# Kernel optimization log

Hardware: AMD Instinct MI355X
Metric: run time of the kernel (lower is better)

Reference implementation:

```python
import jax, jax.numpy as jnp
import numpy as np

DIM = 2048
ORDER = 4
L_MAX = 2048
BATCH = 4  # must equal ORDER due to broadcast in the original module
SEQ = 2048


def setup_inputs() -> dict:
    key = jax.random.key(0)
    k1, k2 = jax.random.split(key)
    x = jax.random.normal(k1, (BATCH, DIM, SEQ), dtype=jnp.float32)
    kernel = jax.random.normal(k2, (ORDER, DIM, L_MAX), dtype=jnp.float32) * 0.02
    bias = jnp.zeros((DIM,), dtype=jnp.float32)
    return {"x": x, "kernel": kernel, "bias": bias}


def reference(x, kernel, bias):
    # x: (B, dim, L); kernel: (order, dim, l_max); B == order by broadcast
    seq_len = x.shape[-1]
    n = 2 * seq_len  # zero-padded FFT length for linear (causal) convolution
    x_fft = jnp.fft.rfft(x, n=n, axis=-1)            # (B, dim, n//2+1) complex
    kernel_fft = jnp.fft.rfft(kernel, n=n, axis=-1)  # (order, dim, n//2+1)
    y_fft = x_fft * kernel_fft                       # broadcast: B == order
    y = jnp.fft.irfft(y_fft, n=n, axis=-1)[:, :, :seq_len]
    return y + x + bias[None, :, None]
```

## Files before the change

kernel.cpp:

```cpp
#include <hip/hip_runtime.h>

typedef __attribute__((ext_vector_type(8)))  short short8;
typedef __attribute__((ext_vector_type(16))) float f32x16;

#define SEQ    2048
#define XPITCH 20
#define XROWS  96
#define XSZ    (XROWS * XPITCH)
#define KSZ    1044
#define WSZ    (XSZ + 2 * KSZ)

__device__ inline unsigned int pack_bf16_2(float lo, float hi) {
    unsigned int ul = __float_as_uint(lo);
    unsigned int uh = __float_as_uint(hi);
    ul = (ul + 0x7fffu + ((ul >> 16) & 1u)) >> 16;
    uh = (uh + 0x7fffu + ((uh >> 16) & 1u)) >> 16;
    return (ul & 0xffffu) | (uh << 16);
}

#define MFMA(A, B, C) __builtin_amdgcn_mfma_f32_32x32x16_bf16( \
    __builtin_bit_cast(short8, A), __builtin_bit_cast(short8, B), C, 0, 0, 0)

__global__ __launch_bounds__(256, 2)
void hyena_mfma(const float* __restrict__ x, const float* __restrict__ kern,
                const float* __restrict__ bias, float* __restrict__ out)
{
    __shared__ __align__(16) unsigned int lds[4 * WSZ];

    const int tid = threadIdx.x;
    const int wid = tid >> 6;
    const int l   = tid & 63;
    const int n   = l & 31;
    const int hi  = l >> 5;
    const int row = blockIdx.x * 4 + wid;
    const size_t rb = (size_t)row * SEQ;

    unsigned int* xld  = lds + wid * WSZ;
    unsigned int* bufA = xld + XSZ;
    unsigned int* bufB = bufA + KSZ;

    #pragma unroll
    for (int it = 0; it < 16; ++it) {
        const int e = it * 128 + 2 * l;
        float2 v = *(const float2*)&x[rb + e];
        const int R = 32 + (e >> 5);
        xld[R * XPITCH + ((e & 31) >> 1)] = pack_bf16_2(v.x, v.y);
    }
    #pragma unroll
    for (int it = 0; it < 10; ++it) xld[it * 64 + l] = 0u;

    #pragma unroll
    for (int it = 0; it < 16; ++it) {
        const int j = it * 128 + 2 * l;
        float2 v = *(const float2*)&kern[rb + (2046 - j)];
        bufA[j >> 1] = pack_bf16_2(v.y, v.x);
    }
    if (l < 20) bufA[1024 + l] = 0u;
    __syncthreads();

    #pragma unroll
    for (int it = 0; it < 17; ++it) {
        const int m = it * 64 + l;
        if (m < 1040) {
            unsigned int a = bufA[m], b = bufA[m + 1];
            bufB[m] = (a >> 16) | (b << 16);
        }
    }
    __syncthreads();

    int iA = (32 + n) * XPITCH + 4 * hi;
    const int base0 = 2047 - n + 8 * hi;
    const unsigned int* kb;
    int iK;
    if (base0 & 1) { kb = bufB; iK = (base0 - 1) >> 1; }
    else           { kb = bufA; iK = base0 >> 1; }

    f32x16 acc0 = {}, acc1a = {}, acc1b = {};

    #pragma unroll 4
    for (int r = 0; r < 32; ++r) {
        const uint4 a00 = *(const uint4*)(xld + iA);
        const uint4 a01 = *(const uint4*)(xld + iA + 8);
        const uint4 a10 = *(const uint4*)(xld + iA + 32 * XPITCH);
        const uint4 a11 = *(const uint4*)(xld + iA + 32 * XPITCH + 8);
        uint4 b00, b01, b10, b11;
        b00.x = kb[iK];       b00.y = kb[iK + 1];   b00.z = kb[iK + 2];   b00.w = kb[iK + 3];
        b01.x = kb[iK + 8];   b01.y = kb[iK + 9];   b01.z = kb[iK + 10];  b01.w = kb[iK + 11];
        b10.x = kb[iK - 512]; b10.y = kb[iK - 511]; b10.z = kb[iK - 510]; b10.w = kb[iK - 509];
        b11.x = kb[iK - 504]; b11.y = kb[iK - 503]; b11.z = kb[iK - 502]; b11.w = kb[iK - 501];

        acc0  = MFMA(a00, b00, acc0);
        acc0  = MFMA(a01, b01, acc0);
        acc1a = MFMA(a10, b00, acc1a);
        acc1a = MFMA(a11, b01, acc1a);
        acc1b = MFMA(a00, b10, acc1b);
        acc1b = MFMA(a01, b11, acc1b);

        iA -= XPITCH;
        iK -= 16;
    }

    const float bv = bias[row & 2047];
    #pragma unroll
    for (int mt = 0; mt < 2; ++mt) {
        #pragma unroll
        for (int t = 0; t < 16; ++t) {
            const int rloc = (t & 3) + 8 * (t >> 2) + 4 * hi;
            const int p = mt * 32 + rloc;
            const unsigned int w = xld[(32 + p) * XPITCH + (n >> 1)];
            const float xr = __uint_as_float((n & 1) ? (w & 0xffff0000u) : (w << 16));
            const float a = mt ? (acc1a[t] + acc1b[t]) : acc0[t];
            out[rb + (size_t)p * 32 + n] = a + xr + bv;
        }
    }
}

extern "C" void kernel_launch(void* const* d_in, const int* in_sizes, int n_in,
                              void* d_out, int out_size, void* d_ws, size_t ws_size,
                              hipStream_t stream) {
    const float* x    = (const float*)d_in[0];
    const float* kern = (const float*)d_in[1];
    const float* bias = (const float*)d_in[2];
    float* out = (float*)d_out;

    hipLaunchKernelGGL(hyena_mfma, dim3(2048), dim3(256), 0, stream,
                       x, kern, bias, out);
}
```

Before: 69.54 us.

## Drop shifted kernel copy, realign B operands via funnel shifts, raise occupancy

Removes the second, half-element-shifted copy of the reversed kernel and the 32 zero-padding rows of x from shared memory. Misaligned B fragments are now built in registers with 64-bit funnel shifts and selects, and zero A rows come from a small shared zero region chosen per lane. This cuts per-block shared memory and one barrier, so launch bounds are raised to 4 blocks per CU. The cost is extra ALU work and more LDS loads per MFMA step in the inner loop, and lower register headroom at the higher occupancy.

```diff
diff --git a/kernel.cpp b/kernel.cpp
--- a/kernel.cpp
+++ b/kernel.cpp
@@ -2,17 +2,19 @@
 
 typedef __attribute__((ext_vector_type(8)))  short short8;
 typedef __attribute__((ext_vector_type(16))) float f32x16;
+typedef unsigned int uint;
+typedef unsigned long long ull;
 
 #define SEQ    2048
 #define XPITCH 20
-#define XROWS  96
-#define XSZ    (XROWS * XPITCH)
-#define KSZ    1044
-#define WSZ    (XSZ + 2 * KSZ)
+#define XSZ    (64 * XPITCH)
+#define KSZ    1040
+#define WSZ    (XSZ + KSZ)
+#define LDSU   (4 * WSZ + 16)
 
-__device__ inline unsigned int pack_bf16_2(float lo, float hi) {
-    unsigned int ul = __float_as_uint(lo);
-    unsigned int uh = __float_as_uint(hi);
+__device__ inline uint pack_bf16_2(float lo, float hi) {
+    uint ul = __float_as_uint(lo);
+    uint uh = __float_as_uint(hi);
     ul = (ul + 0x7fffu + ((ul >> 16) & 1u)) >> 16;
     uh = (uh + 0x7fffu + ((uh >> 16) & 1u)) >> 16;
     return (ul & 0xffffu) | (uh << 16);
@@ -21,11 +23,23 @@
 #define MFMA(A, B, C) __builtin_amdgcn_mfma_f32_32x32x16_bf16( \
     __builtin_bit_cast(short8, A), __builtin_bit_cast(short8, B), C, 0, 0, 0)
 
-__global__ __launch_bounds__(256, 2)
+__device__ inline uint fnl(uint h, uint l, uint sh) {
+    return (uint)((((ull)h << 32) | l) >> sh);
+}
+
+#define SEL4(W0, W1, W2, W3, W4, W5, OUT) {                          \
+    uint t0 = c2 ? (W1) : (W0), t1 = c2 ? (W2) : (W1),               \
+         t2 = c2 ? (W3) : (W2), t3 = c2 ? (W4) : (W3),               \
+         t4 = c2 ? (W5) : (W4);                                      \
+    OUT.x = fnl(t1, t0, sh); OUT.y = fnl(t2, t1, sh);                \
+    OUT.z = fnl(t3, t2, sh); OUT.w = fnl(t4, t3, sh); }
+
+__global__ __launch_bounds__(256, 4)
 void hyena_mfma(const float* __restrict__ x, const float* __restrict__ kern,
                 const float* __restrict__ bias, float* __restrict__ out)
 {
-    __shared__ __align__(16) unsigned int lds[4 * WSZ];
+    __shared__ __align__(16) uint lds[LDSU];
+    char* ldsb = (char*)lds;
 
     const int tid = threadIdx.x;
     const int wid = tid >> 6;
@@ -35,69 +49,69 @@
     const int row = blockIdx.x * 4 + wid;
     const size_t rb = (size_t)row * SEQ;
 
-    unsigned int* xld  = lds + wid * WSZ;
-    unsigned int* bufA = xld + XSZ;
-    unsigned int* bufB = bufA + KSZ;
+    uint* xw = lds + wid * WSZ;
+    uint* kw = xw + XSZ;
 
     #pragma unroll
     for (int it = 0; it < 16; ++it) {
         const int e = it * 128 + 2 * l;
         float2 v = *(const float2*)&x[rb + e];
-        const int R = 32 + (e >> 5);
-        xld[R * XPITCH + ((e & 31) >> 1)] = pack_bf16_2(v.x, v.y);
+        xw[(e >> 5) * XPITCH + ((e & 31) >> 1)] = pack_bf16_2(v.x, v.y);
     }
-    #pragma unroll
-    for (int it = 0; it < 10; ++it) xld[it * 64 + l] = 0u;
-
     #pragma unroll
     for (int it = 0; it < 16; ++it) {
         const int j = it * 128 + 2 * l;
         float2 v = *(const float2*)&kern[rb + (2046 - j)];
-        bufA[j >> 1] = pack_bf16_2(v.y, v.x);
+        kw[j >> 1] = pack_bf16_2(v.y, v.x);
     }
-    if (l < 20) bufA[1024 + l] = 0u;
+    if (l < 16) kw[1024 + l] = 0u;
+    if (tid < 16) lds[4 * WSZ + tid] = 0u;
     __syncthreads();
 
-    #pragma unroll
-    for (int it = 0; it < 17; ++it) {
-        const int m = it * 64 + l;
-        if (m < 1040) {
-            unsigned int a = bufA[m], b = bufA[m + 1];
-            bufB[m] = (a >> 16) | (b << 16);
-        }
-    }
-    __syncthreads();
-
-    int iA = (32 + n) * XPITCH + 4 * hi;
-    const int base0 = 2047 - n + 8 * hi;
-    const unsigned int* kb;
-    int iK;
-    if (base0 & 1) { kb = bufB; iK = (base0 - 1) >> 1; }
-    else           { kb = bufA; iK = base0 >> 1; }
+    const int st00 = 2047 - n + 8 * hi;
+    const bool c2  = (st00 & 2) != 0;
+    const uint sh  = (uint)(st00 & 1) << 4;
+    int vk  = (wid * WSZ + XSZ) * 4 + ((st00 & ~3) << 1) - 2048;
+    int va2 = wid * WSZ * 4 + (n + 32) * 80 + 16 * hi;
+    const int vz = 4 * WSZ * 4 + 16 * hi;
 
     f32x16 acc0 = {}, acc1a = {}, acc1b = {};
 
-    #pragma unroll 4
+    #pragma unroll 2
     for (int r = 0; r < 32; ++r) {
-        const uint4 a00 = *(const uint4*)(xld + iA);
-        const uint4 a01 = *(const uint4*)(xld + iA + 8);
-        const uint4 a10 = *(const uint4*)(xld + iA + 32 * XPITCH);
-        const uint4 a11 = *(const uint4*)(xld + iA + 32 * XPITCH + 8);
-        uint4 b00, b01, b10, b11;
-        b00.x = kb[iK];       b00.y = kb[iK + 1];   b00.z = kb[iK + 2];   b00.w = kb[iK + 3];
-        b01.x = kb[iK + 8];   b01.y = kb[iK + 9];   b01.z = kb[iK + 10];  b01.w = kb[iK + 11];
-        b10.x = kb[iK - 512]; b10.y = kb[iK - 511]; b10.z = kb[iK - 510]; b10.w = kb[iK - 509];
-        b11.x = kb[iK - 504]; b11.y = kb[iK - 503]; b11.z = kb[iK - 502]; b11.w = kb[iK - 501];
+        const int va = (n >= r) ? (va2 - 2560) : vz;
+        const uint4 a00 = *(const uint4*)(ldsb + va);
+        const uint4 a01 = *(const uint4*)(ldsb + va + 32);
+        const uint4 a10 = *(const uint4*)(ldsb + va2);
+        const uint4 a11 = *(const uint4*)(ldsb + va2 + 32);
 
-        acc0  = MFMA(a00, b00, acc0);
-        acc0  = MFMA(a01, b01, acc0);
-        acc1a = MFMA(a10, b00, acc1a);
-        acc1a = MFMA(a11, b01, acc1a);
-        acc1b = MFMA(a00, b10, acc1b);
-        acc1b = MFMA(a01, b11, acc1b);
+        uint2 q0, q1, q2;
+        uint4 B;
+        q0 = *(const uint2*)(ldsb + vk + 2048);
+        q1 = *(const uint2*)(ldsb + vk + 2056);
+        q2 = *(const uint2*)(ldsb + vk + 2064);
+        SEL4(q0.x, q0.y, q1.x, q1.y, q2.x, q2.y, B);
+        acc0  = MFMA(a00, B, acc0);
+        acc1a = MFMA(a10, B, acc1a);
+        q0 = *(const uint2*)(ldsb + vk + 2080);
+        q1 = *(const uint2*)(ldsb + vk + 2088);
+        q2 = *(const uint2*)(ldsb + vk + 2096);
+        SEL4(q0.x, q0.y, q1.x, q1.y, q2.x, q2.y, B);
+        acc0  = MFMA(a01, B, acc0);
+        acc1a = MFMA(a11, B, acc1a);
+        q0 = *(const uint2*)(ldsb + vk);
+        q1 = *(const uint2*)(ldsb + vk + 8);
+        q2 = *(const uint2*)(ldsb + vk + 16);
+        SEL4(q0.x, q0.y, q1.x, q1.y, q2.x, q2.y, B);
+        acc1b = MFMA(a00, B, acc1b);
+        q0 = *(const uint2*)(ldsb + vk + 32);
+        q1 = *(const uint2*)(ldsb + vk + 40);
+        q2 = *(const uint2*)(ldsb + vk + 48);
+        SEL4(q0.x, q0.y, q1.x, q1.y, q2.x, q2.y, B);
+        acc1b = MFMA(a01, B, acc1b);
 
-        iA -= XPITCH;
-        iK -= 16;
+        va2 -= 80;
+        vk  -= 64;
     }
 
     const float bv = bias[row & 2047];
@@ -107,7 +121,7 @@
         for (int t = 0; t < 16; ++t) {
             const int rloc = (t & 3) + 8 * (t >> 2) + 4 * hi;
             const int p = mt * 32 + rloc;
-            const unsigned int w = xld[(32 + p) * XPITCH + (n >> 1)];
+            const uint w = xw[p * XPITCH + (n >> 1)];
             const float xr = __uint_as_float((n & 1) ? (w & 0xffff0000u) : (w << 16));
             const float a = mt ? (acc1a[t] + acc1b[t]) : acc0[t];
             out[rb + (size_t)p * 32 + n] = a + xr + bv;
```

Result: slower. 74.60 us (+7.3%).
